# Kernel tuning notes

Measured on AMD Instinct MI355X. Metric: run time of the kernel, lower is better.

The kernel has to match this reference:

```python
import jax, jax.numpy as jnp
import numpy as np

BLOCK = 128
QMAX = 127.0


def act_quant(x2d):
    # Per (row, 128-wide block) symmetric int8 quantization.
    # x2d: [M, K] -> q int8-valued [M, K], scales [M, K//BLOCK]
    M, K = x2d.shape
    xb = x2d.reshape(M, K // BLOCK, BLOCK)
    s = jnp.max(jnp.abs(xb), axis=-1) / QMAX            # [M, K//BLOCK]
    s = jnp.maximum(s, 1e-12)
    q = jnp.clip(jnp.round(xb / s[..., None]), -128.0, 127.0)
    return q, s  # q kept in fp32 (exact small ints)


def weight_quant(w):
    # w: [N, K] -> q [N, K], scales [N//BLOCK, K//BLOCK]
    N, K = w.shape
    wb = w.reshape(N // BLOCK, BLOCK, K // BLOCK, BLOCK)
    s = jnp.max(jnp.abs(wb), axis=(1, 3)) / QMAX        # [N//BLOCK, K//BLOCK]
    s = jnp.maximum(s, 1e-12)
    q = jnp.clip(jnp.round(wb / s[:, None, :, None]), -128.0, 127.0)
    return q.reshape(N, K), s


def setup_inputs() -> dict:
    key = jax.random.key(0)
    k1, k2, k3 = jax.random.split(key, 3)
    x = jax.random.normal(k1, (4, 2048, 4096), dtype=jnp.float32)
    weight = jax.random.normal(k2, (4096, 4096), dtype=jnp.float32) * 0.02
    bias = jax.random.normal(k3, (4096,), dtype=jnp.float32) * 0.02
    return {"x": x, "weight": weight, "bias": bias}


def reference(x, weight, bias):
    # Int8Linear.forward: block-quantize activation, int8 GEMM with
    # grouped dequant scales (equivalent to dequantize-then-matmul), add bias.
    orig_shape = x.shape
    K = weight.shape[1]
    N = weight.shape[0]
    x2d = x.reshape(-1, K)                              # [M, K]
    M = x2d.shape[0]

    xq, xs = act_quant(x2d)                             # [M,Kb,128], [M,Kb]
    wq, ws = weight_quant(weight)                       # [N,K],     [Nb,Kb]

    # Dequantize (exact factorization of the scaled int8 GEMM):
    # out[m,n] = sum_kb xs[m,kb]*ws[nb,kb] * sum_c xq[m,kb,c]*wq[n,kb,c]
    x_dq = (xq * xs[..., None]).reshape(M, K)
    wqb = wq.reshape(N // BLOCK, BLOCK, K // BLOCK, BLOCK)
    w_dq = (wqb * ws[:, None, :, None]).reshape(N, K)

    out = x_dq @ w_dq.T + bias                          # [M, N]
    return out.reshape(orig_shape[:-1] + (N,))
```

## Files before the change

### kernel.cpp

```cpp
#include <hip/hip_runtime.h>
#include <stdint.h>

#define K_DIM 4096
#define N_DIM 4096
#define KB    32
#define QMAXF 127.0f

typedef int v4i __attribute__((ext_vector_type(4)));

__device__ __forceinline__ void async_copy16(void* lds, const void* gptr) {
    __builtin_amdgcn_global_load_lds(
        (__attribute__((address_space(1))) void*)gptr,
        (__attribute__((address_space(3))) void*)lds, 16, 0, 0);
}

__global__ __launch_bounds__(256) void act_quant_kernel(
    const float* __restrict__ x, int8_t* __restrict__ xq,
    float* __restrict__ xs_t, int M)
{
    const int m = blockIdx.x;
    const int t = threadIdx.x;
    const float* xrow = x + (size_t)m * K_DIM;
    int8_t* qrow = xq + (size_t)m * K_DIM;

#pragma unroll
    for (int p = 0; p < 4; ++p) {
        const int base = p * 1024 + t * 4;
        float4 v = *(const float4*)(xrow + base);
        float a = fmaxf(fmaxf(fabsf(v.x), fabsf(v.y)), fmaxf(fabsf(v.z), fabsf(v.w)));
#pragma unroll
        for (int off = 1; off < 32; off <<= 1)
            a = fmaxf(a, __shfl_xor(a, off, 64));
        const float s = fmaxf(a / QMAXF, 1e-12f);
        const float inv = 1.0f / s;
        float q0 = fminf(fmaxf(rintf(v.x * inv), -128.f), 127.f);
        float q1 = fminf(fmaxf(rintf(v.y * inv), -128.f), 127.f);
        float q2 = fminf(fmaxf(rintf(v.z * inv), -128.f), 127.f);
        float q3 = fminf(fmaxf(rintf(v.w * inv), -128.f), 127.f);
        char4 pk;
        pk.x = (char)(int)q0; pk.y = (char)(int)q1;
        pk.z = (char)(int)q2; pk.w = (char)(int)q3;
        *(char4*)(qrow + base) = pk;
        if ((t & 31) == 0) {
            const int g = base >> 7;
            xs_t[(size_t)g * M + m] = s;
        }
    }
}

__global__ __launch_bounds__(256) void weight_quant_kernel(
    const float* __restrict__ w, int8_t* __restrict__ wq, float* __restrict__ ws)
{
    const int nb = blockIdx.x >> 5;
    const int kb = blockIdx.x & 31;
    const int t  = threadIdx.x;
    const int n0 = nb * 128, k0 = kb * 128;

    float4 vals[16];
    float a = 0.f;
#pragma unroll
    for (int ii = 0; ii < 16; ++ii) {
        const int e = ii * 1024 + t * 4;
        const int row = e >> 7, col = e & 127;
        float4 v = *(const float4*)(w + (size_t)(n0 + row) * K_DIM + k0 + col);
        vals[ii] = v;
        a = fmaxf(a, fmaxf(fmaxf(fabsf(v.x), fabsf(v.y)), fmaxf(fabsf(v.z), fabsf(v.w))));
    }
#pragma unroll
    for (int off = 1; off < 64; off <<= 1)
        a = fmaxf(a, __shfl_xor(a, off, 64));
    __shared__ float wred[4];
    if ((t & 63) == 0) wred[t >> 6] = a;
    __syncthreads();
    a = fmaxf(fmaxf(wred[0], wred[1]), fmaxf(wred[2], wred[3]));
    const float s = fmaxf(a / QMAXF, 1e-12f);
    const float inv = 1.0f / s;
    if (t == 0) ws[nb * KB + kb] = s;

#pragma unroll
    for (int ii = 0; ii < 16; ++ii) {
        const int e = ii * 1024 + t * 4;
        const int row = e >> 7, col = e & 127;
        float4 v = vals[ii];
        char4 pk;
        pk.x = (char)(int)fminf(fmaxf(rintf(v.x * inv), -128.f), 127.f);
        pk.y = (char)(int)fminf(fmaxf(rintf(v.y * inv), -128.f), 127.f);
        pk.z = (char)(int)fminf(fmaxf(rintf(v.z * inv), -128.f), 127.f);
        pk.w = (char)(int)fminf(fmaxf(rintf(v.w * inv), -128.f), 127.f);
        *(char4*)(wq + (size_t)(n0 + row) * K_DIM + k0 + col) = pk;
    }
}

__global__ __launch_bounds__(256, 3) void gemm_kernel(
    const int8_t* __restrict__ xq, const int8_t* __restrict__ wq,
    const float* __restrict__ xs_t, const float* __restrict__ ws,
    const float* __restrict__ bias, float* __restrict__ out, int M)
{
    __shared__ __align__(16) int8_t As[128 * 128];
    __shared__ __align__(16) int8_t Bs[128 * 128];
    __shared__ __align__(16) float  xs_s[KB * 128];
    __shared__ float ws_s[KB];

    const int t    = threadIdx.x;
    const int lane = t & 63;
    const int wave = t >> 6;
    const int nb   = blockIdx.x;
    const int n0   = nb * 128;
    const int m0   = blockIdx.y * 128;

#pragma unroll
    for (int i = 0; i < 4; ++i) {
        const int idx = t * 4 + i * 1024;
        const int kbi = idx >> 7, r = idx & 127;
        *(float4*)&xs_s[idx] = *(const float4*)&xs_t[(size_t)kbi * M + m0 + r];
    }
    if (t < KB) ws_s[t] = ws[nb * KB + t];

    const int wm    = (wave >> 1) * 64;
    const int wn    = (wave & 1) * 64;
    const int frow  = lane & 15;
    const int q     = lane >> 4;
    const int quad4 = q * 4;
    const int sw0   = ((q ^ (frow & 7)) * 16);

    float4 facc[4][4] = {};

    float bj[4];
#pragma unroll
    for (int j = 0; j < 4; ++j) bj[j] = bias[n0 + wn + j * 16 + frow];

    for (int kb = 0; kb < KB; ++kb) {
        __syncthreads();
        const int8_t* Ag = xq + (size_t)m0 * K_DIM + kb * 128;
        const int8_t* Bg = wq + (size_t)n0 * K_DIM + kb * 128;
#pragma unroll
        for (int it = 0; it < 4; ++it) {
            const int ci  = it * 256 + t;
            const int row = ci >> 3;
            const int c   = (ci & 7) ^ (row & 7);
            void* la = (void*)&As[(it * 256 + wave * 64) * 16];
            void* lb = (void*)&Bs[(it * 256 + wave * 64) * 16];
            async_copy16(la, Ag + (size_t)row * K_DIM + c * 16);
            async_copy16(lb, Bg + (size_t)row * K_DIM + c * 16);
        }
        __syncthreads();

        v4i a0[4], a1[4], b0[4], b1[4];
#pragma unroll
        for (int i = 0; i < 4; ++i) {
            a0[i] = *(const v4i*)&As[(wm + i * 16 + frow) * 128 + sw0];
            a1[i] = *(const v4i*)&As[(wm + i * 16 + frow) * 128 + (sw0 ^ 64)];
            b0[i] = *(const v4i*)&Bs[(wn + i * 16 + frow) * 128 + sw0];
            b1[i] = *(const v4i*)&Bs[(wn + i * 16 + frow) * 128 + (sw0 ^ 64)];
        }
        const float wskb = ws_s[kb];
#pragma unroll
        for (int i = 0; i < 4; ++i) {
            float4 xs4 = *(const float4*)&xs_s[kb * 128 + wm + i * 16 + quad4];
            const float s0 = xs4.x * wskb, s1 = xs4.y * wskb;
            const float s2 = xs4.z * wskb, s3 = xs4.w * wskb;
#pragma unroll
            for (int j = 0; j < 4; ++j) {
                v4i d = __builtin_amdgcn_mfma_i32_16x16x64_i8(a0[i], b0[j], (v4i){0, 0, 0, 0}, 0, 0, 0);
                d = __builtin_amdgcn_mfma_i32_16x16x64_i8(a1[i], b1[j], d, 0, 0, 0);
                facc[i][j].x += (float)d[0] * s0;
                facc[i][j].y += (float)d[1] * s1;
                facc[i][j].z += (float)d[2] * s2;
                facc[i][j].w += (float)d[3] * s3;
            }
        }
    }

#pragma unroll
    for (int i = 0; i < 4; ++i) {
#pragma unroll
        for (int r = 0; r < 4; ++r) {
            const int row = m0 + wm + i * 16 + quad4 + r;
            float* orow = out + (size_t)row * N_DIM + n0 + wn + frow;
#pragma unroll
            for (int j = 0; j < 4; ++j)
                orow[j * 16] = ((const float*)&facc[i][j])[r] + bj[j];
        }
    }
}

extern "C" void kernel_launch(void* const* d_in, const int* in_sizes, int n_in,
                              void* d_out, int out_size, void* d_ws, size_t ws_size,
                              hipStream_t stream)
{
    const float* x    = (const float*)d_in[0];
    const float* w    = (const float*)d_in[1];
    const float* bias = (const float*)d_in[2];
    float* out = (float*)d_out;
    const int M = in_sizes[0] / K_DIM;

    int8_t* xq  = (int8_t*)d_ws;
    int8_t* wqp = xq + (size_t)M * K_DIM;
    float*  xst = (float*)(wqp + (size_t)N_DIM * K_DIM);
    float*  wsp = xst + (size_t)KB * M;

    act_quant_kernel<<<M, 256, 0, stream>>>(x, xq, xst, M);
    weight_quant_kernel<<<(N_DIM / 128) * KB, 256, 0, stream>>>(w, wqp, wsp);
    gemm_kernel<<<dim3(N_DIM / 128, M / 128), 256, 0, stream>>>(
        xq, wqp, xst, wsp, bias, out, M);
}
```

Before: 432.6 us.

## Rewrite int8 GEMM as 256x256 double-buffered tile with phased MFMA scheduling

Result: slower. 502.2 us (+16.1%).

```diff
diff --git a/kernel.cpp b/kernel.cpp
--- a/kernel.cpp
+++ b/kernel.cpp
@@ -91,88 +91,164 @@
     }
 }
 
-__global__ __launch_bounds__(256, 3) void gemm_kernel(
+__global__ __launch_bounds__(512, 2) void gemm_kernel(
     const int8_t* __restrict__ xq, const int8_t* __restrict__ wq,
     const float* __restrict__ xs_t, const float* __restrict__ ws,
     const float* __restrict__ bias, float* __restrict__ out, int M)
 {
-    __shared__ __align__(16) int8_t As[128 * 128];
-    __shared__ __align__(16) int8_t Bs[128 * 128];
-    __shared__ __align__(16) float  xs_s[KB * 128];
-    __shared__ float ws_s[KB];
+    __shared__ __align__(16) int8_t As[2][256 * 128];
+    __shared__ __align__(16) int8_t Bs[2][256 * 128];
 
     const int t    = threadIdx.x;
     const int lane = t & 63;
     const int wave = t >> 6;
-    const int nb   = blockIdx.x;
-    const int n0   = nb * 128;
-    const int m0   = blockIdx.y * 128;
-
-#pragma unroll
-    for (int i = 0; i < 4; ++i) {
-        const int idx = t * 4 + i * 1024;
-        const int kbi = idx >> 7, r = idx & 127;
-        *(float4*)&xs_s[idx] = *(const float4*)&xs_t[(size_t)kbi * M + m0 + r];
-    }
-    if (t < KB) ws_s[t] = ws[nb * KB + t];
-
-    const int wm    = (wave >> 1) * 64;
-    const int wn    = (wave & 1) * 64;
+
+    const int nwg  = gridDim.x;
+    const int cpx  = nwg >> 3;
+    const int bid  = blockIdx.x;
+    const int tile = (bid & 7) * cpx + (bid >> 3);
+    const int nbt  = tile & 15;
+    const int mbt  = tile >> 4;
+    const int n0   = nbt * 256;
+    const int m0   = mbt * 256;
+
+    const int wm    = (wave >> 2) * 128;
+    const int wn    = (wave & 3) * 64;
     const int frow  = lane & 15;
     const int q     = lane >> 4;
     const int quad4 = q * 4;
-    const int sw0   = ((q ^ (frow & 7)) * 16);
-
-    float4 facc[4][4] = {};
+    const int sw0   = (q ^ (frow & 7)) * 16;
+    const int wsrow = ((n0 + wn) >> 7) * KB;
+
+    int st_row[4], st_c[4];
+#pragma unroll
+    for (int it = 0; it < 4; ++it) {
+        const int ci = it * 512 + t;
+        st_row[it] = ci >> 3;
+        st_c[it]   = (ci & 7) ^ (st_row[it] & 7);
+    }
+
+    float4 facc[8][4] = {};
 
     float bj[4];
 #pragma unroll
     for (int j = 0; j < 4; ++j) bj[j] = bias[n0 + wn + j * 16 + frow];
 
+    {
+        const int8_t* Ag = xq + (size_t)m0 * K_DIM;
+        const int8_t* Bg = wq + (size_t)n0 * K_DIM;
+#pragma unroll
+        for (int it = 0; it < 4; ++it) {
+            async_copy16(&As[0][(it * 512 + wave * 64) * 16],
+                         Ag + (size_t)st_row[it] * K_DIM + st_c[it] * 16);
+            async_copy16(&Bs[0][(it * 512 + wave * 64) * 16],
+                         Bg + (size_t)st_row[it] * K_DIM + st_c[it] * 16);
+        }
+        asm volatile("s_waitcnt vmcnt(0)" ::: "memory");
+        __builtin_amdgcn_s_barrier();
+    }
+
+#define PH_PRE  do { __builtin_amdgcn_s_barrier(); \
+                     asm volatile("s_waitcnt lgkmcnt(0)" ::: "memory"); \
+                     __builtin_amdgcn_sched_barrier(0); \
+                     __builtin_amdgcn_s_setprio(1); } while (0)
+#define PH_POST do { __builtin_amdgcn_s_setprio(0); \
+                     __builtin_amdgcn_s_barrier(); } while (0)
+
+#define READ_A(ihb) \
+    _Pragma("unroll") \
+    for (int i = 0; i < 4; ++i) { \
+        const int r = wm + ((ihb) + i) * 16 + frow; \
+        a0[i] = *(const v4i*)&As[cur][r * 128 + sw0]; \
+        a1[i] = *(const v4i*)&As[cur][r * 128 + (sw0 ^ 64)]; \
+    }
+#define READ_B(jb) \
+    _Pragma("unroll") \
+    for (int j = 0; j < 2; ++j) { \
+        const int r = wn + ((jb) + j) * 16 + frow; \
+        b0[j] = *(const v4i*)&Bs[cur][r * 128 + sw0]; \
+        b1[j] = *(const v4i*)&Bs[cur][r * 128 + (sw0 ^ 64)]; \
+    }
+#define READ_XS(ihb) \
+    _Pragma("unroll") \
+    for (int i = 0; i < 4; ++i) \
+        xs4[i] = *(const float4*)&xs_t[(size_t)kb * M + m0 + wm + ((ihb) + i) * 16 + quad4];
+#define MFMA_QUAD(ihb, jb) \
+    _Pragma("unroll") \
+    for (int i = 0; i < 4; ++i) { \
+        const float s0 = xs4[i].x * wskb, s1 = xs4[i].y * wskb; \
+        const float s2 = xs4[i].z * wskb, s3 = xs4[i].w * wskb; \
+        _Pragma("unroll") \
+        for (int j = 0; j < 2; ++j) { \
+            v4i d = __builtin_amdgcn_mfma_i32_16x16x64_i8(a0[i], b0[j], (v4i){0, 0, 0, 0}, 0, 0, 0); \
+            d = __builtin_amdgcn_mfma_i32_16x16x64_i8(a1[i], b1[j], d, 0, 0, 0); \
+            float4& f = facc[(ihb) + i][(jb) + j]; \
+            f.x += (float)d[0] * s0; \
+            f.y += (float)d[1] * s1; \
+            f.z += (float)d[2] * s2; \
+            f.w += (float)d[3] * s3; \
+        } \
+    }
+
     for (int kb = 0; kb < KB; ++kb) {
-        __syncthreads();
-        const int8_t* Ag = xq + (size_t)m0 * K_DIM + kb * 128;
-        const int8_t* Bg = wq + (size_t)n0 * K_DIM + kb * 128;
-#pragma unroll
-        for (int it = 0; it < 4; ++it) {
-            const int ci  = it * 256 + t;
-            const int row = ci >> 3;
-            const int c   = (ci & 7) ^ (row & 7);
-            void* la = (void*)&As[(it * 256 + wave * 64) * 16];
-            void* lb = (void*)&Bs[(it * 256 + wave * 64) * 16];
-            async_copy16(la, Ag + (size_t)row * K_DIM + c * 16);
-            async_copy16(lb, Bg + (size_t)row * K_DIM + c * 16);
-        }
-        __syncthreads();
-
-        v4i a0[4], a1[4], b0[4], b1[4];
-#pragma unroll
-        for (int i = 0; i < 4; ++i) {
-            a0[i] = *(const v4i*)&As[(wm + i * 16 + frow) * 128 + sw0];
-            a1[i] = *(const v4i*)&As[(wm + i * 16 + frow) * 128 + (sw0 ^ 64)];
-            b0[i] = *(const v4i*)&Bs[(wn + i * 16 + frow) * 128 + sw0];
-            b1[i] = *(const v4i*)&Bs[(wn + i * 16 + frow) * 128 + (sw0 ^ 64)];
-        }
-        const float wskb = ws_s[kb];
-#pragma unroll
-        for (int i = 0; i < 4; ++i) {
-            float4 xs4 = *(const float4*)&xs_s[kb * 128 + wm + i * 16 + quad4];
-            const float s0 = xs4.x * wskb, s1 = xs4.y * wskb;
-            const float s2 = xs4.z * wskb, s3 = xs4.w * wskb;
-#pragma unroll
-            for (int j = 0; j < 4; ++j) {
-                v4i d = __builtin_amdgcn_mfma_i32_16x16x64_i8(a0[i], b0[j], (v4i){0, 0, 0, 0}, 0, 0, 0);
-                d = __builtin_amdgcn_mfma_i32_16x16x64_i8(a1[i], b1[j], d, 0, 0, 0);
-                facc[i][j].x += (float)d[0] * s0;
-                facc[i][j].y += (float)d[1] * s1;
-                facc[i][j].z += (float)d[2] * s2;
-                facc[i][j].w += (float)d[3] * s3;
-            }
-        }
-    }
-
-#pragma unroll
-    for (int i = 0; i < 4; ++i) {
+        const int cur = kb & 1;
+        const int nxt = cur ^ 1;
+        const int pre = (kb + 1 < KB);
+        const float wskb = ws[__builtin_amdgcn_readfirstlane(wsrow + kb)];
+        const int8_t* Agn = xq + (size_t)m0 * K_DIM + (size_t)(kb + 1) * 128;
+        const int8_t* Bgn = wq + (size_t)n0 * K_DIM + (size_t)(kb + 1) * 128;
+
+        v4i a0[4], a1[4], b0[2], b1[2];
+        float4 xs4[4];
+
+        READ_A(0)
+        READ_B(0)
+        READ_XS(0)
+        if (pre) {
+#pragma unroll
+            for (int it = 0; it < 4; ++it)
+                async_copy16(&As[nxt][(it * 512 + wave * 64) * 16],
+                             Agn + (size_t)st_row[it] * K_DIM + st_c[it] * 16);
+        }
+        PH_PRE;
+        MFMA_QUAD(0, 0)
+        PH_POST;
+
+        READ_B(2)
+        if (pre) {
+#pragma unroll
+            for (int it = 0; it < 4; ++it)
+                async_copy16(&Bs[nxt][(it * 512 + wave * 64) * 16],
+                             Bgn + (size_t)st_row[it] * K_DIM + st_c[it] * 16);
+        }
+        PH_PRE;
+        MFMA_QUAD(0, 2)
+        PH_POST;
+
+        READ_A(4)
+        READ_B(0)
+        READ_XS(4)
+        PH_PRE;
+        MFMA_QUAD(4, 0)
+        PH_POST;
+
+        READ_B(2)
+        PH_PRE;
+        MFMA_QUAD(4, 2)
+        __builtin_amdgcn_s_setprio(0);
+        asm volatile("s_waitcnt vmcnt(0)" ::: "memory");
+        __builtin_amdgcn_s_barrier();
+    }
+
+#undef PH_PRE
+#undef PH_POST
+#undef READ_A
+#undef READ_B
+#undef READ_XS
+#undef MFMA_QUAD
+
+#pragma unroll
+    for (int i = 0; i < 8; ++i) {
 #pragma unroll
         for (int r = 0; r < 4; ++r) {
             const int row = m0 + wm + i * 16 + quad4 + r;
@@ -201,6 +277,6 @@
 
     act_quant_kernel<<<M, 256, 0, stream>>>(x, xq, xst, M);
     weight_quant_kernel<<<(N_DIM / 128) * KB, 256, 0, stream>>>(w, wqp, wsp);
-    gemm_kernel<<<dim3(N_DIM / 128, M / 128), 256, 0, stream>>>(
+    gemm_kernel<<<(N_DIM / 256) * (M / 256), 512, 0, stream>>>(
         xq, wqp, xst, wsp, bias, out, M);
 }
```

## Double-buffer GEMM LDS tiles, remap blocks across XCDs, grid-stride act quant

Applied to the files above, without the earlier changes.

Result: slower. 474.9 us (+9.8%).

```diff
diff --git a/kernel.cpp b/kernel.cpp
--- a/kernel.cpp
+++ b/kernel.cpp
@@ -18,32 +18,33 @@
     const float* __restrict__ x, int8_t* __restrict__ xq,
     float* __restrict__ xs_t, int M)
 {
-    const int m = blockIdx.x;
     const int t = threadIdx.x;
-    const float* xrow = x + (size_t)m * K_DIM;
-    int8_t* qrow = xq + (size_t)m * K_DIM;
-
-#pragma unroll
-    for (int p = 0; p < 4; ++p) {
-        const int base = p * 1024 + t * 4;
-        float4 v = *(const float4*)(xrow + base);
-        float a = fmaxf(fmaxf(fabsf(v.x), fabsf(v.y)), fmaxf(fabsf(v.z), fabsf(v.w)));
-#pragma unroll
-        for (int off = 1; off < 32; off <<= 1)
-            a = fmaxf(a, __shfl_xor(a, off, 64));
-        const float s = fmaxf(a / QMAXF, 1e-12f);
-        const float inv = 1.0f / s;
-        float q0 = fminf(fmaxf(rintf(v.x * inv), -128.f), 127.f);
-        float q1 = fminf(fmaxf(rintf(v.y * inv), -128.f), 127.f);
-        float q2 = fminf(fmaxf(rintf(v.z * inv), -128.f), 127.f);
-        float q3 = fminf(fmaxf(rintf(v.w * inv), -128.f), 127.f);
-        char4 pk;
-        pk.x = (char)(int)q0; pk.y = (char)(int)q1;
-        pk.z = (char)(int)q2; pk.w = (char)(int)q3;
-        *(char4*)(qrow + base) = pk;
-        if ((t & 31) == 0) {
-            const int g = base >> 7;
-            xs_t[(size_t)g * M + m] = s;
+    for (int m = blockIdx.x; m < M; m += gridDim.x) {
+        const float* xrow = x + (size_t)m * K_DIM;
+        int8_t* qrow = xq + (size_t)m * K_DIM;
+
+#pragma unroll
+        for (int p = 0; p < 4; ++p) {
+            const int base = p * 1024 + t * 4;
+            float4 v = *(const float4*)(xrow + base);
+            float a = fmaxf(fmaxf(fabsf(v.x), fabsf(v.y)), fmaxf(fabsf(v.z), fabsf(v.w)));
+#pragma unroll
+            for (int off = 1; off < 32; off <<= 1)
+                a = fmaxf(a, __shfl_xor(a, off, 64));
+            const float s = fmaxf(a / QMAXF, 1e-12f);
+            const float inv = 1.0f / s;
+            float q0 = fminf(fmaxf(rintf(v.x * inv), -128.f), 127.f);
+            float q1 = fminf(fmaxf(rintf(v.y * inv), -128.f), 127.f);
+            float q2 = fminf(fmaxf(rintf(v.z * inv), -128.f), 127.f);
+            float q3 = fminf(fmaxf(rintf(v.w * inv), -128.f), 127.f);
+            char4 pk;
+            pk.x = (char)(int)q0; pk.y = (char)(int)q1;
+            pk.z = (char)(int)q2; pk.w = (char)(int)q3;
+            *(char4*)(qrow + base) = pk;
+            if ((t & 31) == 0) {
+                const int g = base >> 7;
+                xs_t[(size_t)g * M + m] = s;
+            }
         }
     }
 }
@@ -91,74 +92,99 @@
     }
 }
 
-__global__ __launch_bounds__(256, 3) void gemm_kernel(
+__global__ __launch_bounds__(256, 2) void gemm_kernel(
     const int8_t* __restrict__ xq, const int8_t* __restrict__ wq,
     const float* __restrict__ xs_t, const float* __restrict__ ws,
     const float* __restrict__ bias, float* __restrict__ out, int M)
 {
-    __shared__ __align__(16) int8_t As[128 * 128];
-    __shared__ __align__(16) int8_t Bs[128 * 128];
-    __shared__ __align__(16) float  xs_s[KB * 128];
-    __shared__ float ws_s[KB];
+    __shared__ __align__(16) int8_t As[2][128 * 128];
+    __shared__ __align__(16) int8_t Bs[2][128 * 128];
+    __shared__ __align__(16) float  xs_lds[2][128];
 
     const int t    = threadIdx.x;
     const int lane = t & 63;
     const int wave = t >> 6;
-    const int nb   = blockIdx.x;
-    const int n0   = nb * 128;
-    const int m0   = blockIdx.y * 128;
-
-#pragma unroll
-    for (int i = 0; i < 4; ++i) {
-        const int idx = t * 4 + i * 1024;
-        const int kbi = idx >> 7, r = idx & 127;
-        *(float4*)&xs_s[idx] = *(const float4*)&xs_t[(size_t)kbi * M + m0 + r];
-    }
-    if (t < KB) ws_s[t] = ws[nb * KB + t];
+
+    const int nwg  = gridDim.x;
+    const int cpx  = nwg >> 3;
+    const int bid  = blockIdx.x;
+    const int tile = (bid & 7) * cpx + (bid >> 3);
+    const int nbt  = tile & 31;
+    const int mbt  = tile >> 5;
+    const int n0   = nbt * 128;
+    const int m0   = mbt * 128;
 
     const int wm    = (wave >> 1) * 64;
     const int wn    = (wave & 1) * 64;
     const int frow  = lane & 15;
     const int q     = lane >> 4;
     const int quad4 = q * 4;
-    const int sw0   = ((q ^ (frow & 7)) * 16);
+    const int sw0   = (q ^ (frow & 7)) * 16;
+    const int wsrow = nbt * KB;
+
+    int st_off[4];
+#pragma unroll
+    for (int it = 0; it < 4; ++it) {
+        const int ci  = it * 256 + t;
+        const int row = ci >> 3;
+        const int c   = (ci & 7) ^ (row & 7);
+        st_off[it] = row * K_DIM + c * 16;
+    }
+
+    const int8_t* Abase = xq + (size_t)m0 * K_DIM;
+    const int8_t* Bbase = wq + (size_t)n0 * K_DIM;
 
     float4 facc[4][4] = {};
 
-    float bj[4];
-#pragma unroll
-    for (int j = 0; j < 4; ++j) bj[j] = bias[n0 + wn + j * 16 + frow];
+#pragma unroll
+    for (int it = 0; it < 4; ++it) {
+        async_copy16(&As[0][(it * 256 + wave * 64) * 16], Abase + st_off[it]);
+        async_copy16(&Bs[0][(it * 256 + wave * 64) * 16], Bbase + st_off[it]);
+    }
+    if (t < 32)
+        async_copy16(&xs_lds[0][0], xs_t + m0 + t * 4);
+    __syncthreads();
 
     for (int kb = 0; kb < KB; ++kb) {
-        __syncthreads();
-        const int8_t* Ag = xq + (size_t)m0 * K_DIM + kb * 128;
-        const int8_t* Bg = wq + (size_t)n0 * K_DIM + kb * 128;
-#pragma unroll
-        for (int it = 0; it < 4; ++it) {
-            const int ci  = it * 256 + t;
-            const int row = ci >> 3;
-            const int c   = (ci & 7) ^ (row & 7);
-            void* la = (void*)&As[(it * 256 + wave * 64) * 16];
-            void* lb = (void*)&Bs[(it * 256 + wave * 64) * 16];
-            async_copy16(la, Ag + (size_t)row * K_DIM + c * 16);
-            async_copy16(lb, Bg + (size_t)row * K_DIM + c * 16);
-        }
-        __syncthreads();
+        const int cur = kb & 1;
+        const int nxt = cur ^ 1;
+
+        if (kb + 1 < KB) {
+            const int8_t* Agn = Abase + (size_t)(kb + 1) * 128;
+            const int8_t* Bgn = Bbase + (size_t)(kb + 1) * 128;
+#pragma unroll
+            for (int it = 0; it < 4; ++it) {
+                async_copy16(&As[nxt][(it * 256 + wave * 64) * 16], Agn + st_off[it]);
+                async_copy16(&Bs[nxt][(it * 256 + wave * 64) * 16], Bgn + st_off[it]);
+            }
+            if (t < 32)
+                async_copy16(&xs_lds[nxt][0], xs_t + (size_t)(kb + 1) * M + m0 + t * 4);
+        }
+
+        const float wskb = ws[wsrow + kb];
 
         v4i a0[4], a1[4], b0[4], b1[4];
+        float4 xs4[4];
 #pragma unroll
         for (int i = 0; i < 4; ++i) {
-            a0[i] = *(const v4i*)&As[(wm + i * 16 + frow) * 128 + sw0];
-            a1[i] = *(const v4i*)&As[(wm + i * 16 + frow) * 128 + (sw0 ^ 64)];
-            b0[i] = *(const v4i*)&Bs[(wn + i * 16 + frow) * 128 + sw0];
-            b1[i] = *(const v4i*)&Bs[(wn + i * 16 + frow) * 128 + (sw0 ^ 64)];
-        }
-        const float wskb = ws_s[kb];
+            const int r = (wm + i * 16 + frow) * 128;
+            a0[i] = *(const v4i*)&As[cur][r + sw0];
+            a1[i] = *(const v4i*)&As[cur][r + (sw0 ^ 64)];
+        }
+#pragma unroll
+        for (int j = 0; j < 4; ++j) {
+            const int r = (wn + j * 16 + frow) * 128;
+            b0[j] = *(const v4i*)&Bs[cur][r + sw0];
+            b1[j] = *(const v4i*)&Bs[cur][r + (sw0 ^ 64)];
+        }
+#pragma unroll
+        for (int i = 0; i < 4; ++i)
+            xs4[i] = *(const float4*)&xs_lds[cur][wm + i * 16 + quad4];
+
 #pragma unroll
         for (int i = 0; i < 4; ++i) {
-            float4 xs4 = *(const float4*)&xs_s[kb * 128 + wm + i * 16 + quad4];
-            const float s0 = xs4.x * wskb, s1 = xs4.y * wskb;
-            const float s2 = xs4.z * wskb, s3 = xs4.w * wskb;
+            const float s0 = xs4[i].x * wskb, s1 = xs4[i].y * wskb;
+            const float s2 = xs4[i].z * wskb, s3 = xs4[i].w * wskb;
 #pragma unroll
             for (int j = 0; j < 4; ++j) {
                 v4i d = __builtin_amdgcn_mfma_i32_16x16x64_i8(a0[i], b0[j], (v4i){0, 0, 0, 0}, 0, 0, 0);
@@ -169,8 +195,13 @@
                 facc[i][j].w += (float)d[3] * s3;
             }
         }
-    }
-
+
+        __syncthreads();
+    }
+
+    float bj[4];
+#pragma unroll
+    for (int j = 0; j < 4; ++j) bj[j] = bias[n0 + wn + j * 16 + frow];
 #pragma unroll
     for (int i = 0; i < 4; ++i) {
 #pragma unroll
@@ -199,8 +230,8 @@
     float*  xst = (float*)(wqp + (size_t)N_DIM * K_DIM);
     float*  wsp = xst + (size_t)KB * M;
 
-    act_quant_kernel<<<M, 256, 0, stream>>>(x, xq, xst, M);
+    act_quant_kernel<<<2048, 256, 0, stream>>>(x, xq, xst, M);
     weight_quant_kernel<<<(N_DIM / 128) * KB, 256, 0, stream>>>(w, wqp, wsp);
-    gemm_kernel<<<dim3(N_DIM / 128, M / 128), 256, 0, stream>>>(
+    gemm_kernel<<<(N_DIM / 128) * (M / 128), 256, 0, stream>>>(
         xq, wqp, xst, wsp, bias, out, M);
 }
```
